# Kernel optimization log

Hardware: AMD Instinct MI355X
Metric: run time of the kernel (lower is better)

Reference implementation:

```python
import jax, jax.numpy as jnp
import numpy as np

N_NODES = 100000
N_EDGES = 1600000
IN_FEATS = 256
OUT_FEATS = 128


def setup_inputs() -> dict:
    key = jax.random.key(0)
    k1, k2, k3, k4, k5 = jax.random.split(key, 5)
    x = jax.random.normal(k1, (N_NODES, IN_FEATS), dtype=jnp.float32)
    edge_row = jax.random.randint(k2, (N_EDGES,), 0, N_NODES, dtype=jnp.int64 if jax.config.jax_enable_x64 else jnp.int32)
    edge_col = jax.random.randint(k3, (N_EDGES,), 0, N_NODES, dtype=jnp.int64 if jax.config.jax_enable_x64 else jnp.int32)
    edge_val = jax.random.uniform(k4, (N_EDGES,), dtype=jnp.float32)
    # xavier_uniform-like init for weight
    limit = float(np.sqrt(6.0 / (IN_FEATS + OUT_FEATS)))
    weight = jax.random.uniform(k5, (IN_FEATS, OUT_FEATS), dtype=jnp.float32, minval=-limit, maxval=limit)
    b = jnp.zeros((OUT_FEATS,), dtype=jnp.float32)
    return {"x": x, "edge_row": edge_row, "edge_col": edge_col, "edge_val": edge_val, "weight": weight, "b": b}


def reference(x, edge_row, edge_col, edge_val, weight, b):
    # sup = input @ weight : [N, out_feats]
    sup = x @ weight
    # out = spmm(adj, sup): gather source rows, scale by edge value, scatter-add to dest
    msgs = edge_val[:, None] * sup[edge_col]          # [E, out_feats]
    out = jax.ops.segment_sum(msgs, edge_row, num_segments=N_NODES)  # [N, out_feats]
    return out + b
```

## Files before the change

kernel.cpp:

```cpp
#include <hip/hip_runtime.h>


#define K_FEATS 256
#define N_FEATS 128
#define BSHIFT 7
#define BROWS 128
#define BCAP 3072
#define CHUNK 8192
#define EPT 32
#define RMOD 5

typedef __attribute__((ext_vector_type(8))) short short8;
typedef __attribute__((ext_vector_type(4))) float float4v;

__device__ __forceinline__ unsigned short f2bf(float f) {
    unsigned int u = __float_as_uint(f);
    unsigned int r = u + 0x7FFF + ((u >> 16) & 1);
    return (unsigned short)(r >> 16);
}

__global__ __launch_bounds__(256) void prep_w(const float* __restrict__ w,
                                              unsigned short* __restrict__ wt) {
    int n = blockIdx.x;
    int k = threadIdx.x;
    wt[n * K_FEATS + k] = f2bf(w[k * N_FEATS + n]);
}

__global__ __launch_bounds__(256) void zero_ints(int* __restrict__ p, int n) {
    int i = blockIdx.x * 256 + threadIdx.x;
    if (i < n) p[i] = 0;
}

__global__ __launch_bounds__(256) void gemm_partition(
        const float* __restrict__ x, const unsigned short* __restrict__ wt,
        unsigned short* __restrict__ sup, int M, int NT,
        const int* __restrict__ erow, const int* __restrict__ ecol,
        const float* __restrict__ eval_, int* __restrict__ bcur,
        int2* __restrict__ tmp, int E, int NB, int NCH) {
    __shared__ int hist[1024];
    __shared__ int cur[1024];
    const int g   = blockIdx.x;
    const int tid = threadIdx.x;

    if (g % RMOD == 0) {
        int pid = g / RMOD;
        if (pid >= NCH) return;
        const long e0 = (long)pid * CHUNK;

        for (int i = tid; i < NB; i += 256) hist[i] = 0;
        __syncthreads();

        int rows[EPT];
#pragma unroll
        for (int i = 0; i < EPT; i++) {
            long e = e0 + tid + i * 256;
            int r = -1;
            if (e < E) {
                r = erow[e];
                atomicAdd(&hist[r >> BSHIFT], 1);
            }
            rows[i] = r;
        }
        __syncthreads();

        for (int i = tid; i < NB; i += 256) {
            int c = hist[i];
            cur[i] = c ? atomicAdd(&bcur[i], c) : 0;
        }
        __syncthreads();

#pragma unroll
        for (int i = 0; i < EPT; i++) {
            long e = e0 + tid + i * 256;
            if (e >= E) continue;
            int r = rows[i];
            int b = r >> BSHIFT;
            int p = atomicAdd(&cur[b], 1);
            if (p < BCAP)
                tmp[(long)b * BCAP + p] = make_int2(((r & (BROWS - 1)) << 17) | ecol[e],
                                                    __float_as_int(eval_[e]));
        }
        return;
    }

    int tile = g - g / RMOD - 1;
    if (tile >= NT) return;

    const int wv   = tid >> 6;
    const int lane = tid & 63;
    const int l15  = lane & 15;
    const int quad = lane >> 4;
    const int row0 = tile * 128 + wv * 32;

    float4v acc[2][8];
#pragma unroll
    for (int mt = 0; mt < 2; mt++)
#pragma unroll
        for (int nt = 0; nt < 8; nt++) acc[mt][nt] = (float4v)(0.f);

#pragma unroll 2
    for (int k0 = 0; k0 < K_FEATS; k0 += 32) {
        short8 afrag[2];
#pragma unroll
        for (int mt = 0; mt < 2; mt++) {
            int grow = row0 + mt * 16 + l15;
            float4 a0 = make_float4(0.f, 0.f, 0.f, 0.f);
            float4 a1 = make_float4(0.f, 0.f, 0.f, 0.f);
            if (grow < M) {
                const float* p = x + (long)grow * K_FEATS + k0 + quad * 8;
                a0 = *(const float4*)p;
                a1 = *(const float4*)(p + 4);
            }
            short8 af;
            af[0] = (short)f2bf(a0.x); af[1] = (short)f2bf(a0.y);
            af[2] = (short)f2bf(a0.z); af[3] = (short)f2bf(a0.w);
            af[4] = (short)f2bf(a1.x); af[5] = (short)f2bf(a1.y);
            af[6] = (short)f2bf(a1.z); af[7] = (short)f2bf(a1.w);
            afrag[mt] = af;
        }
        short8 bfrag[8];
#pragma unroll
        for (int nt = 0; nt < 8; nt++) {
            bfrag[nt] = *(const short8*)(wt + (nt * 16 + l15) * K_FEATS + k0 + quad * 8);
        }
#pragma unroll
        for (int mt = 0; mt < 2; mt++)
#pragma unroll
            for (int nt = 0; nt < 8; nt++)
                acc[mt][nt] = __builtin_amdgcn_mfma_f32_16x16x32_bf16(
                    afrag[mt], bfrag[nt], acc[mt][nt], 0, 0, 0);
    }

#pragma unroll
    for (int mt = 0; mt < 2; mt++) {
#pragma unroll
        for (int reg = 0; reg < 4; reg++) {
            int grow = row0 + mt * 16 + quad * 4 + reg;
            if (grow < M) {
#pragma unroll
                for (int nt = 0; nt < 8; nt++) {
                    sup[(long)grow * N_FEATS + nt * 16 + l15] = f2bf(acc[mt][nt][reg]);
                }
            }
        }
    }
}

__global__ __launch_bounds__(1024) void bucket_scan(const int* __restrict__ bcnt,
                                                    int* __restrict__ bbase,
                                                    int* __restrict__ off0,
                                                    int NB, int M) {
    __shared__ int sm[1024];
    int t = threadIdx.x;
    int v = 0;
    if (t < NB) { v = bcnt[t]; if (v > BCAP) v = BCAP; }
    sm[t] = v;
    __syncthreads();
#pragma unroll
    for (int s = 1; s < 1024; s <<= 1) {
        int a = (t >= s) ? sm[t - s] : 0;
        __syncthreads();
        sm[t] += a;
        __syncthreads();
    }
    if (t < NB) bbase[t] = sm[t] - v;
    if (t == 1023) off0[M] = sm[1023];
}

__global__ __launch_bounds__(256) void bucket_to_sorted(const int* __restrict__ bcnt,
                                                        const int* __restrict__ bbase,
                                                        const int2* __restrict__ tmp,
                                                        int* __restrict__ off0,
                                                        int2* __restrict__ sedge, int M) {
    __shared__ int hist[BROWS];
    __shared__ int cur[BROWS];
    const int b   = blockIdx.x;
    const int tid = threadIdx.x;
    const int row0 = b << BSHIFT;

    if (tid < BROWS) hist[tid] = 0;
    __syncthreads();

    int cnt = bcnt[b];
    if (cnt > BCAP) cnt = BCAP;
    const int2* t = tmp + (long)b * BCAP;

    for (int i = tid; i < cnt; i += 256)
        atomicAdd(&hist[(unsigned)t[i].x >> 17], 1);
    __syncthreads();

    if (tid < BROWS) cur[tid] = hist[tid];
    __syncthreads();
#pragma unroll
    for (int s = 1; s < BROWS; s <<= 1) {
        int v = 0;
        if (tid >= s && tid < BROWS) v = cur[tid - s];
        __syncthreads();
        if (tid < BROWS) cur[tid] += v;
        __syncthreads();
    }

    const int base = bbase[b];
    if (tid < BROWS) {
        int start = base + cur[tid] - hist[tid];
        cur[tid] = start;
        if (row0 + tid < M) off0[row0 + tid] = start;
    }
    __syncthreads();

    for (int i = tid; i < cnt; i += 256) {
        int2 e = t[i];
        int rl = (unsigned)e.x >> 17;
        int p = atomicAdd(&cur[rl], 1);
        sedge[p] = make_int2(e.x & 0x1FFFF, e.y);
    }
}

__global__ __launch_bounds__(256) void gcn_spmm(const int* __restrict__ off0,
                                                const int2* __restrict__ sedge,
                                                const unsigned short* __restrict__ sup,
                                                const float* __restrict__ b,
                                                float* __restrict__ out, int M) {
    int row  = blockIdx.x * 4 + (threadIdx.x >> 6);
    if (row >= M) return;
    int lane = threadIdx.x & 63;
    int half = lane >> 5;
    int l31  = lane & 31;
    int s = off0[row], e = off0[row + 1];
    const uint2* sup64 = (const uint2*)sup;

    float4v acc = (float4v)(0.f);
    int base = s;
    for (; base + 8 <= e; base += 8) {
        int2 ed[4];
#pragma unroll
        for (int u = 0; u < 4; u++) ed[u] = sedge[base + half + 2 * u];
        uint2 g[4];
#pragma unroll
        for (int u = 0; u < 4; u++) g[u] = sup64[(long)ed[u].x * 32 + l31];
#pragma unroll
        for (int u = 0; u < 4; u++) {
            float v = __int_as_float(ed[u].y);
            acc.x += v * __uint_as_float(g[u].x << 16);
            acc.y += v * __uint_as_float(g[u].x & 0xFFFF0000u);
            acc.z += v * __uint_as_float(g[u].y << 16);
            acc.w += v * __uint_as_float(g[u].y & 0xFFFF0000u);
        }
    }
    for (int i = base + half; i < e; i += 2) {
        int2 ed = sedge[i];
        uint2 g = sup64[(long)ed.x * 32 + l31];
        float v = __int_as_float(ed.y);
        acc.x += v * __uint_as_float(g.x << 16);
        acc.y += v * __uint_as_float(g.x & 0xFFFF0000u);
        acc.z += v * __uint_as_float(g.y << 16);
        acc.w += v * __uint_as_float(g.y & 0xFFFF0000u);
    }

    acc.x += __shfl_xor(acc.x, 32);
    acc.y += __shfl_xor(acc.y, 32);
    acc.z += __shfl_xor(acc.z, 32);
    acc.w += __shfl_xor(acc.w, 32);

    if (half == 0) {
        float4v bb = ((const float4v*)b)[l31];
        acc += bb;
        *(float4v*)(out + (long)row * N_FEATS + l31 * 4) = acc;
    }
}

extern "C" void kernel_launch(void* const* d_in, const int* in_sizes, int n_in,
                              void* d_out, int out_size, void* d_ws, size_t ws_size,
                              hipStream_t stream) {
    const float* x     = (const float*)d_in[0];
    const int*   erow  = (const int*)d_in[1];
    const int*   ecol  = (const int*)d_in[2];
    const float* eval_ = (const float*)d_in[3];
    const float* w     = (const float*)d_in[4];
    const float* b     = (const float*)d_in[5];
    float* out = (float*)d_out;

    const int M  = in_sizes[0] / K_FEATS;
    const int E  = in_sizes[1];
    const int NB = (M + BROWS - 1) >> BSHIFT;
    const int NT = (M + 127) / 128;
    const int NCH = (E + CHUNK - 1) / CHUNK;

    size_t o_sup   = 0;
    size_t o_wt    = o_sup   + (((size_t)M * N_FEATS * 2 + 15) & ~15ul);
    size_t o_off0  = o_wt    + (size_t)K_FEATS * N_FEATS * 2;
    size_t o_bcur  = o_off0  + (((size_t)(M + 1) * 4 + 15) & ~15ul);
    size_t o_bbase = o_bcur  + (((size_t)NB * 4 + 15) & ~15ul);
    size_t o_tmp   = o_bbase + (((size_t)NB * 4 + 15) & ~15ul);
    size_t o_edge  = o_tmp   + ((size_t)NB * BCAP * 8);

    unsigned short* sup   = (unsigned short*)((char*)d_ws + o_sup);
    unsigned short* wt    = (unsigned short*)((char*)d_ws + o_wt);
    int*            off0  = (int*)((char*)d_ws + o_off0);
    int*            bcur  = (int*)((char*)d_ws + o_bcur);
    int*            bbase = (int*)((char*)d_ws + o_bbase);
    int2*           tmp   = (int2*)((char*)d_ws + o_tmp);
    int2*           sedge = (int2*)((char*)d_ws + o_edge);

    prep_w<<<N_FEATS, 256, 0, stream>>>(w, wt);
    zero_ints<<<(NB + 255) / 256, 256, 0, stream>>>(bcur, NB);

    int nblk = NT + NCH;
    gemm_partition<<<nblk, 256, 0, stream>>>(x, wt, sup, M, NT,
                                             erow, ecol, eval_, bcur, tmp, E, NB, NCH);

    bucket_scan<<<1, 1024, 0, stream>>>(bcur, bbase, off0, NB, M);
    bucket_to_sorted<<<NB, 256, 0, stream>>>(bcur, bbase, tmp, off0, sedge, M);

    gcn_spmm<<<(M + 3) / 4, 256, 0, stream>>>(off0, sedge, sup, b, out, M);
}
```

Baseline: 329.3 us.

## Replace bucketed two-pass CSR build with per-row histogram, scan, and atomic scatter

Replaces the row-bucket partitioning (LDS histogram, bucket temp buffer, per-bucket local sort) with a per-row global atomic histogram computed alongside the GEMM, a two-kernel prefix scan, and a direct atomic scatter into CSR order. This drops the intermediate bucket buffer and its extra read/write pass, but adds global atomics on 100k counters and non-deterministic edge order within rows. The GEMM also prefetches the next K-slice of x one iteration ahead and uses the packed v_cvt_pk_bf16_f32 instruction for bf16 conversion. Weight prep and counter zeroing are merged into one launch.

```diff
diff --git a/kernel.cpp b/kernel.cpp
--- a/kernel.cpp
+++ b/kernel.cpp
@@ -3,9 +3,6 @@
 
 #define K_FEATS 256
 #define N_FEATS 128
-#define BSHIFT 7
-#define BROWS 128
-#define BCAP 3072
 #define CHUNK 8192
 #define EPT 32
 #define RMOD 5
@@ -19,26 +16,29 @@
     return (unsigned short)(r >> 16);
 }
 
-__global__ __launch_bounds__(256) void prep_w(const float* __restrict__ w,
-                                              unsigned short* __restrict__ wt) {
-    int n = blockIdx.x;
-    int k = threadIdx.x;
-    wt[n * K_FEATS + k] = f2bf(w[k * N_FEATS + n]);
-}
-
-__global__ __launch_bounds__(256) void zero_ints(int* __restrict__ p, int n) {
-    int i = blockIdx.x * 256 + threadIdx.x;
-    if (i < n) p[i] = 0;
-}
-
-__global__ __launch_bounds__(256) void gemm_partition(
+__device__ __forceinline__ unsigned int cvt_pk_bf16(float lo, float hi) {
+    unsigned int r;
+    asm("v_cvt_pk_bf16_f32 %0, %1, %2" : "=v"(r) : "v"(lo), "v"(hi));
+    return r;
+}
+
+__global__ __launch_bounds__(256) void prep_zero(const float* __restrict__ w,
+                                                 unsigned short* __restrict__ wt,
+                                                 int* __restrict__ rcnt, int M) {
+    int g = blockIdx.x;
+    if (g < N_FEATS) {
+        int k = threadIdx.x;
+        wt[g * K_FEATS + k] = f2bf(w[k * N_FEATS + g]);
+        return;
+    }
+    int i = (g - N_FEATS) * 256 + threadIdx.x;
+    if (i < M) rcnt[i] = 0;
+}
+
+__global__ __launch_bounds__(256) void gemm_hist(
         const float* __restrict__ x, const unsigned short* __restrict__ wt,
         unsigned short* __restrict__ sup, int M, int NT,
-        const int* __restrict__ erow, const int* __restrict__ ecol,
-        const float* __restrict__ eval_, int* __restrict__ bcur,
-        int2* __restrict__ tmp, int E, int NB, int NCH) {
-    __shared__ int hist[1024];
-    __shared__ int cur[1024];
+        const int* __restrict__ erow, int* __restrict__ rcnt, int E, int NCH) {
     const int g   = blockIdx.x;
     const int tid = threadIdx.x;
 
@@ -46,39 +46,10 @@
         int pid = g / RMOD;
         if (pid >= NCH) return;
         const long e0 = (long)pid * CHUNK;
-
-        for (int i = tid; i < NB; i += 256) hist[i] = 0;
-        __syncthreads();
-
-        int rows[EPT];
 #pragma unroll
         for (int i = 0; i < EPT; i++) {
             long e = e0 + tid + i * 256;
-            int r = -1;
-            if (e < E) {
-                r = erow[e];
-                atomicAdd(&hist[r >> BSHIFT], 1);
-            }
-            rows[i] = r;
-        }
-        __syncthreads();
-
-        for (int i = tid; i < NB; i += 256) {
-            int c = hist[i];
-            cur[i] = c ? atomicAdd(&bcur[i], c) : 0;
-        }
-        __syncthreads();
-
-#pragma unroll
-        for (int i = 0; i < EPT; i++) {
-            long e = e0 + tid + i * 256;
-            if (e >= E) continue;
-            int r = rows[i];
-            int b = r >> BSHIFT;
-            int p = atomicAdd(&cur[b], 1);
-            if (p < BCAP)
-                tmp[(long)b * BCAP + p] = make_int2(((r & (BROWS - 1)) << 17) | ecol[e],
-                                                    __float_as_int(eval_[e]));
+            if (e < E) atomicAdd(&rcnt[erow[e]], 1);
         }
         return;
     }
@@ -98,30 +69,49 @@
 #pragma unroll
         for (int nt = 0; nt < 8; nt++) acc[mt][nt] = (float4v)(0.f);
 
+    float4 ca[2][2];
+#pragma unroll
+    for (int mt = 0; mt < 2; mt++) {
+        int grow = row0 + mt * 16 + l15;
+        ca[mt][0] = make_float4(0.f, 0.f, 0.f, 0.f);
+        ca[mt][1] = make_float4(0.f, 0.f, 0.f, 0.f);
+        if (grow < M) {
+            const float* p = x + (long)grow * K_FEATS + quad * 8;
+            ca[mt][0] = *(const float4*)p;
+            ca[mt][1] = *(const float4*)(p + 4);
+        }
+    }
+
 #pragma unroll 2
     for (int k0 = 0; k0 < K_FEATS; k0 += 32) {
-        short8 afrag[2];
-#pragma unroll
-        for (int mt = 0; mt < 2; mt++) {
-            int grow = row0 + mt * 16 + l15;
-            float4 a0 = make_float4(0.f, 0.f, 0.f, 0.f);
-            float4 a1 = make_float4(0.f, 0.f, 0.f, 0.f);
-            if (grow < M) {
-                const float* p = x + (long)grow * K_FEATS + k0 + quad * 8;
-                a0 = *(const float4*)p;
-                a1 = *(const float4*)(p + 4);
-            }
-            short8 af;
-            af[0] = (short)f2bf(a0.x); af[1] = (short)f2bf(a0.y);
-            af[2] = (short)f2bf(a0.z); af[3] = (short)f2bf(a0.w);
-            af[4] = (short)f2bf(a1.x); af[5] = (short)f2bf(a1.y);
-            af[6] = (short)f2bf(a1.z); af[7] = (short)f2bf(a1.w);
-            afrag[mt] = af;
-        }
         short8 bfrag[8];
 #pragma unroll
         for (int nt = 0; nt < 8; nt++) {
             bfrag[nt] = *(const short8*)(wt + (nt * 16 + l15) * K_FEATS + k0 + quad * 8);
+        }
+        float4 na[2][2];
+        if (k0 + 32 < K_FEATS) {
+#pragma unroll
+            for (int mt = 0; mt < 2; mt++) {
+                int grow = row0 + mt * 16 + l15;
+                na[mt][0] = make_float4(0.f, 0.f, 0.f, 0.f);
+                na[mt][1] = make_float4(0.f, 0.f, 0.f, 0.f);
+                if (grow < M) {
+                    const float* p = x + (long)grow * K_FEATS + (k0 + 32) + quad * 8;
+                    na[mt][0] = *(const float4*)p;
+                    na[mt][1] = *(const float4*)(p + 4);
+                }
+            }
+        }
+        short8 afrag[2];
+#pragma unroll
+        for (int mt = 0; mt < 2; mt++) {
+            union { short8 s; uint4 u; } cv;
+            cv.u.x = cvt_pk_bf16(ca[mt][0].x, ca[mt][0].y);
+            cv.u.y = cvt_pk_bf16(ca[mt][0].z, ca[mt][0].w);
+            cv.u.z = cvt_pk_bf16(ca[mt][1].x, ca[mt][1].y);
+            cv.u.w = cvt_pk_bf16(ca[mt][1].z, ca[mt][1].w);
+            afrag[mt] = cv.s;
         }
 #pragma unroll
         for (int mt = 0; mt < 2; mt++)
@@ -129,6 +119,11 @@
             for (int nt = 0; nt < 8; nt++)
                 acc[mt][nt] = __builtin_amdgcn_mfma_f32_16x16x32_bf16(
                     afrag[mt], bfrag[nt], acc[mt][nt], 0, 0, 0);
+#pragma unroll
+        for (int mt = 0; mt < 2; mt++) {
+            ca[mt][0] = na[mt][0];
+            ca[mt][1] = na[mt][1];
+        }
     }
 
 #pragma unroll
@@ -146,73 +141,87 @@
     }
 }
 
-__global__ __launch_bounds__(1024) void bucket_scan(const int* __restrict__ bcnt,
-                                                    int* __restrict__ bbase,
-                                                    int* __restrict__ off0,
-                                                    int NB, int M) {
-    __shared__ int sm[1024];
-    int t = threadIdx.x;
-    int v = 0;
-    if (t < NB) { v = bcnt[t]; if (v > BCAP) v = BCAP; }
-    sm[t] = v;
+__global__ __launch_bounds__(256) void scan_partial(const int* __restrict__ rcnt,
+                                                    int* __restrict__ bsum, int M) {
+    __shared__ int sm[256];
+    const int blk = blockIdx.x, t = threadIdx.x;
+    const int base = blk * 1024 + t * 4;
+    int s = 0;
+#pragma unroll
+    for (int j = 0; j < 4; j++) {
+        int i = base + j;
+        if (i < M) s += rcnt[i];
+    }
+    sm[t] = s;
     __syncthreads();
-#pragma unroll
-    for (int s = 1; s < 1024; s <<= 1) {
-        int a = (t >= s) ? sm[t - s] : 0;
+    for (int st = 128; st > 0; st >>= 1) {
+        if (t < st) sm[t] += sm[t + st];
+        __syncthreads();
+    }
+    if (t == 0) bsum[blk] = sm[0];
+}
+
+__global__ __launch_bounds__(256) void scan_final(const int* __restrict__ rcnt,
+                                                  const int* __restrict__ bsum,
+                                                  int* __restrict__ off0,
+                                                  int* __restrict__ cur, int M, int NB1) {
+    __shared__ int pb[128];
+    __shared__ int sm[256];
+    const int blk = blockIdx.x, t = threadIdx.x;
+
+    if (t < 128) pb[t] = (t < NB1) ? bsum[t] : 0;
+    __syncthreads();
+    for (int st = 1; st < 128; st <<= 1) {
+        int v = 0;
+        if (t >= st && t < 128) v = pb[t - st];
+        __syncthreads();
+        if (t < 128) pb[t] += v;
+        __syncthreads();
+    }
+    const int blockBase = (blk == 0) ? 0 : pb[blk - 1];
+
+    const int base = blk * 1024 + t * 4;
+    int v[4];
+    int s = 0;
+#pragma unroll
+    for (int j = 0; j < 4; j++) {
+        int i = base + j;
+        v[j] = (i < M) ? rcnt[i] : 0;
+        s += v[j];
+    }
+    sm[t] = s;
+    __syncthreads();
+    for (int st = 1; st < 256; st <<= 1) {
+        int a = 0;
+        if (t >= st) a = sm[t - st];
         __syncthreads();
         sm[t] += a;
         __syncthreads();
     }
-    if (t < NB) bbase[t] = sm[t] - v;
-    if (t == 1023) off0[M] = sm[1023];
-}
-
-__global__ __launch_bounds__(256) void bucket_to_sorted(const int* __restrict__ bcnt,
-                                                        const int* __restrict__ bbase,
-                                                        const int2* __restrict__ tmp,
-                                                        int* __restrict__ off0,
-                                                        int2* __restrict__ sedge, int M) {
-    __shared__ int hist[BROWS];
-    __shared__ int cur[BROWS];
-    const int b   = blockIdx.x;
-    const int tid = threadIdx.x;
-    const int row0 = b << BSHIFT;
-
-    if (tid < BROWS) hist[tid] = 0;
-    __syncthreads();
-
-    int cnt = bcnt[b];
-    if (cnt > BCAP) cnt = BCAP;
-    const int2* t = tmp + (long)b * BCAP;
-
-    for (int i = tid; i < cnt; i += 256)
-        atomicAdd(&hist[(unsigned)t[i].x >> 17], 1);
-    __syncthreads();
-
-    if (tid < BROWS) cur[tid] = hist[tid];
-    __syncthreads();
-#pragma unroll
-    for (int s = 1; s < BROWS; s <<= 1) {
-        int v = 0;
-        if (tid >= s && tid < BROWS) v = cur[tid - s];
-        __syncthreads();
-        if (tid < BROWS) cur[tid] += v;
-        __syncthreads();
-    }
-
-    const int base = bbase[b];
-    if (tid < BROWS) {
-        int start = base + cur[tid] - hist[tid];
-        cur[tid] = start;
-        if (row0 + tid < M) off0[row0 + tid] = start;
-    }
-    __syncthreads();
-
-    for (int i = tid; i < cnt; i += 256) {
-        int2 e = t[i];
-        int rl = (unsigned)e.x >> 17;
-        int p = atomicAdd(&cur[rl], 1);
-        sedge[p] = make_int2(e.x & 0x1FFFF, e.y);
+    int tb = blockBase + ((t == 0) ? 0 : sm[t - 1]);
+#pragma unroll
+    for (int j = 0; j < 4; j++) {
+        int i = base + j;
+        if (i < M) {
+            off0[i] = tb;
+            cur[i]  = tb;
+            tb += v[j];
+            if (i == M - 1) off0[M] = tb;
+        }
+    }
+}
+
+__global__ __launch_bounds__(256) void csr_scatter(const int* __restrict__ erow,
+                                                   const int* __restrict__ ecol,
+                                                   const float* __restrict__ eval_,
+                                                   int* __restrict__ cur,
+                                                   int2* __restrict__ sedge, int E) {
+    const int gid = blockIdx.x * 256 + threadIdx.x;
+    const int T   = gridDim.x * 256;
+    for (int e = gid; e < E; e += T) {
+        int r = erow[e];
+        int p = atomicAdd(&cur[r], 1);
+        sedge[p] = make_int2(ecol[e], __float_as_int(eval_[e]));
     }
 }
 
@@ -280,37 +289,36 @@
     const float* b     = (const float*)d_in[5];
     float* out = (float*)d_out;
 
-    const int M  = in_sizes[0] / K_FEATS;
-    const int E  = in_sizes[1];
-    const int NB = (M + BROWS - 1) >> BSHIFT;
-    const int NT = (M + 127) / 128;
+    const int M   = in_sizes[0] / K_FEATS;
+    const int E   = in_sizes[1];
+    const int NT  = (M + 127) / 128;
     const int NCH = (E + CHUNK - 1) / CHUNK;
-
-    size_t o_sup   = 0;
-    size_t o_wt    = o_sup   + (((size_t)M * N_FEATS * 2 + 15) & ~15ul);
-    size_t o_off0  = o_wt    + (size_t)K_FEATS * N_FEATS * 2;
-    size_t o_bcur  = o_off0  + (((size_t)(M + 1) * 4 + 15) & ~15ul);
-    size_t o_bbase = o_bcur  + (((size_t)NB * 4 + 15) & ~15ul);
-    size_t o_tmp   = o_bbase + (((size_t)NB * 4 + 15) & ~15ul);
-    size_t o_edge  = o_tmp   + ((size_t)NB * BCAP * 8);
-
-    unsigned short* sup   = (unsigned short*)((char*)d_ws + o_sup);
-    unsigned short* wt    = (unsigned short*)((char*)d_ws + o_wt);
-    int*            off0  = (int*)((char*)d_ws + o_off0);
-    int*            bcur  = (int*)((char*)d_ws + o_bcur);
-    int*            bbase = (int*)((char*)d_ws + o_bbase);
-    int2*           tmp   = (int2*)((char*)d_ws + o_tmp);
+    const int NB1 = (M + 1023) / 1024;
+
+    size_t o_sup  = 0;
+    size_t o_wt   = o_sup  + (((size_t)M * N_FEATS * 2 + 15) & ~15ul);
+    size_t o_off0 = o_wt   + (size_t)K_FEATS * N_FEATS * 2;
+    size_t o_rcnt = o_off0 + (((size_t)(M + 1) * 4 + 15) & ~15ul);
+    size_t o_cur  = o_rcnt + (((size_t)M * 4 + 15) & ~15ul);
+    size_t o_bsum = o_cur  + (((size_t)M * 4 + 15) & ~15ul);
+    size_t o_edge = o_bsum + (((size_t)NB1 * 4 + 15) & ~15ul);
+
+    unsigned short* sup  = (unsigned short*)((char*)d_ws + o_sup);
+    unsigned short* wt   = (unsigned short*)((char*)d_ws + o_wt);
+    int*            off0 = (int*)((char*)d_ws + o_off0);
+    int*            rcnt = (int*)((char*)d_ws + o_rcnt);
+    int*            cur  = (int*)((char*)d_ws + o_cur);
+    int*            bsum = (int*)((char*)d_ws + o_bsum);
     int2*           sedge = (int2*)((char*)d_ws + o_edge);
 
-    prep_w<<<N_FEATS, 256, 0, stream>>>(w, wt);
-    zero_ints<<<(NB + 255) / 256, 256, 0, stream>>>(bcur, NB);
-
-    int nblk = NT + NCH;
-    gemm_partition<<<nblk, 256, 0, stream>>>(x, wt, sup, M, NT,
-                                             erow, ecol, eval_, bcur, tmp, E, NB, NCH);
-
-    bucket_scan<<<1, 1024, 0, stream>>>(bcur, bbase, off0, NB, M);
-    bucket_to_sorted<<<NB, 256, 0, stream>>>(bcur, bbase, tmp, off0, sedge, M);
+    prep_zero<<<N_FEATS + (M + 255) / 256, 256, 0, stream>>>(w, wt, rcnt, M);
+
+    gemm_hist<<<NT + NCH, 256, 0, stream>>>(x, wt, sup, M, NT, erow, rcnt, E, NCH);
+
+    scan_partial<<<NB1, 256, 0, stream>>>(rcnt, bsum, M);
+    scan_final<<<NB1, 256, 0, stream>>>(rcnt, bsum, off0, cur, M, NB1);
+
+    csr_scatter<<<(E + 2047) / 2048, 256, 0, stream>>>(erow, ecol, eval_, cur, sedge, E);
 
     gcn_spmm<<<(M + 3) / 4, 256, 0, stream>>>(off0, sedge, sup, b, out, M);
 }
```

New measurement: 447.7 us. 1.36x slower.

## Fuse bucket scan, local sort and SpMM into one per-bucket kernel

Applied to the files above, without the earlier changes.

Replaces the global bucket scan, the bucket-to-sorted pass and the separate SpMM kernel with a single kernel per 128-row bucket. Each block counting-sorts its edges into shared memory (24 KB LDS) and then runs the gather-scale-sum directly from LDS. This removes two launches, the global sorted-edge write and re-read, and the offset array. The cost is fewer blocks (about 782 of them, each with 4 waves looping over 32 rows), so there is less parallelism to hide gather latency, and occupancy is limited by the LDS footprint.

```diff
diff --git a/kernel.cpp b/kernel.cpp
--- a/kernel.cpp
+++ b/kernel.cpp
@@ -6,6 +6,7 @@
 #define BSHIFT 7
 #define BROWS 128
 #define BCAP 3072
+#define STASH 12
 #define CHUNK 8192
 #define EPT 32
 #define RMOD 5
@@ -146,47 +147,38 @@
     }
 }
 
-__global__ __launch_bounds__(1024) void bucket_scan(const int* __restrict__ bcnt,
-                                                    int* __restrict__ bbase,
-                                                    int* __restrict__ off0,
-                                                    int NB, int M) {
-    __shared__ int sm[1024];
-    int t = threadIdx.x;
-    int v = 0;
-    if (t < NB) { v = bcnt[t]; if (v > BCAP) v = BCAP; }
-    sm[t] = v;
-    __syncthreads();
-#pragma unroll
-    for (int s = 1; s < 1024; s <<= 1) {
-        int a = (t >= s) ? sm[t - s] : 0;
-        __syncthreads();
-        sm[t] += a;
-        __syncthreads();
-    }
-    if (t < NB) bbase[t] = sm[t] - v;
-    if (t == 1023) off0[M] = sm[1023];
-}
-
-__global__ __launch_bounds__(256) void bucket_to_sorted(const int* __restrict__ bcnt,
-                                                        const int* __restrict__ bbase,
-                                                        const int2* __restrict__ tmp,
-                                                        int* __restrict__ off0,
-                                                        int2* __restrict__ sedge, int M) {
+__global__ __launch_bounds__(256) void bucket_spmm(const int* __restrict__ bcnt,
+                                                   const int2* __restrict__ tmp,
+                                                   const unsigned short* __restrict__ sup,
+                                                   const float* __restrict__ b,
+                                                   float* __restrict__ out, int M) {
     __shared__ int hist[BROWS];
+    __shared__ int rs[BROWS];
     __shared__ int cur[BROWS];
-    const int b   = blockIdx.x;
-    const int tid = threadIdx.x;
-    const int row0 = b << BSHIFT;
+    __shared__ __align__(16) int2 se[BCAP];
+    const int bkt  = blockIdx.x;
+    const int tid  = threadIdx.x;
+    const int wv   = tid >> 6;
+    const int lane = tid & 63;
+    const int row0 = bkt << BSHIFT;
 
     if (tid < BROWS) hist[tid] = 0;
     __syncthreads();
 
-    int cnt = bcnt[b];
+    int cnt = bcnt[bkt];
     if (cnt > BCAP) cnt = BCAP;
-    const int2* t = tmp + (long)b * BCAP;
-
-    for (int i = tid; i < cnt; i += 256)
-        atomicAdd(&hist[(unsigned)t[i].x >> 17], 1);
+    const int2* t = tmp + (long)bkt * BCAP;
+
+    int2 stash[STASH];
+#pragma unroll
+    for (int j = 0; j < STASH; j++) {
+        int i = tid + j * 256;
+        if (i < cnt) {
+            int2 e = t[i];
+            stash[j] = e;
+            atomicAdd(&hist[(unsigned)e.x >> 17], 1);
+        }
+    }
     __syncthreads();
 
     if (tid < BROWS) cur[tid] = hist[tid];
@@ -199,73 +191,74 @@
         if (tid < BROWS) cur[tid] += v;
         __syncthreads();
     }
-
-    const int base = bbase[b];
     if (tid < BROWS) {
-        int start = base + cur[tid] - hist[tid];
+        int start = cur[tid] - hist[tid];
+        rs[tid]  = start;
         cur[tid] = start;
-        if (row0 + tid < M) off0[row0 + tid] = start;
-    }
-    __syncthreads();
-
-    for (int i = tid; i < cnt; i += 256) {
-        int2 e = t[i];
-        int rl = (unsigned)e.x >> 17;
-        int p = atomicAdd(&cur[rl], 1);
-        sedge[p] = make_int2(e.x & 0x1FFFF, e.y);
-    }
-}
-
-__global__ __launch_bounds__(256) void gcn_spmm(const int* __restrict__ off0,
-                                                const int2* __restrict__ sedge,
-                                                const unsigned short* __restrict__ sup,
-                                                const float* __restrict__ b,
-                                                float* __restrict__ out, int M) {
-    int row  = blockIdx.x * 4 + (threadIdx.x >> 6);
-    if (row >= M) return;
-    int lane = threadIdx.x & 63;
-    int half = lane >> 5;
-    int l31  = lane & 31;
-    int s = off0[row], e = off0[row + 1];
+    }
+    __syncthreads();
+
+#pragma unroll
+    for (int j = 0; j < STASH; j++) {
+        int i = tid + j * 256;
+        if (i < cnt) {
+            int2 e = stash[j];
+            int rl = (unsigned)e.x >> 17;
+            int p = atomicAdd(&cur[rl], 1);
+            se[p] = make_int2(e.x & 0x1FFFF, e.y);
+        }
+    }
+    __syncthreads();
+
+    const int half = lane >> 5;
+    const int l31  = lane & 31;
     const uint2* sup64 = (const uint2*)sup;
-
-    float4v acc = (float4v)(0.f);
-    int base = s;
-    for (; base + 8 <= e; base += 8) {
-        int2 ed[4];
-#pragma unroll
-        for (int u = 0; u < 4; u++) ed[u] = sedge[base + half + 2 * u];
-        uint2 g[4];
-#pragma unroll
-        for (int u = 0; u < 4; u++) g[u] = sup64[(long)ed[u].x * 32 + l31];
-#pragma unroll
-        for (int u = 0; u < 4; u++) {
-            float v = __int_as_float(ed[u].y);
-            acc.x += v * __uint_as_float(g[u].x << 16);
-            acc.y += v * __uint_as_float(g[u].x & 0xFFFF0000u);
-            acc.z += v * __uint_as_float(g[u].y << 16);
-            acc.w += v * __uint_as_float(g[u].y & 0xFFFF0000u);
-        }
-    }
-    for (int i = base + half; i < e; i += 2) {
-        int2 ed = sedge[i];
-        uint2 g = sup64[(long)ed.x * 32 + l31];
-        float v = __int_as_float(ed.y);
-        acc.x += v * __uint_as_float(g.x << 16);
-        acc.y += v * __uint_as_float(g.x & 0xFFFF0000u);
-        acc.z += v * __uint_as_float(g.y << 16);
-        acc.w += v * __uint_as_float(g.y & 0xFFFF0000u);
-    }
-
-    acc.x += __shfl_xor(acc.x, 32);
-    acc.y += __shfl_xor(acc.y, 32);
-    acc.z += __shfl_xor(acc.z, 32);
-    acc.w += __shfl_xor(acc.w, 32);
-
-    if (half == 0) {
-        float4v bb = ((const float4v*)b)[l31];
-        acc += bb;
-        *(float4v*)(out + (long)row * N_FEATS + l31 * 4) = acc;
+    const float4v bb = ((const float4v*)b)[l31];
+
+    for (int rr = 0; rr < 32; rr++) {
+        int r    = wv * 32 + rr;
+        int grow = row0 + r;
+        if (grow >= M) break;
+        int s  = rs[r];
+        int e2 = s + hist[r];
+
+        float4v acc = (float4v)(0.f);
+        int base = s;
+        for (; base + 8 <= e2; base += 8) {
+            int2 ed[4];
+#pragma unroll
+            for (int u = 0; u < 4; u++) ed[u] = se[base + half + 2 * u];
+            uint2 g[4];
+#pragma unroll
+            for (int u = 0; u < 4; u++) g[u] = sup64[(long)ed[u].x * 32 + l31];
+#pragma unroll
+            for (int u = 0; u < 4; u++) {
+                float v = __int_as_float(ed[u].y);
+                acc.x += v * __uint_as_float(g[u].x << 16);
+                acc.y += v * __uint_as_float(g[u].x & 0xFFFF0000u);
+                acc.z += v * __uint_as_float(g[u].y << 16);
+                acc.w += v * __uint_as_float(g[u].y & 0xFFFF0000u);
+            }
+        }
+        for (int i = base + half; i < e2; i += 2) {
+            int2 ed = se[i];
+            uint2 g = sup64[(long)ed.x * 32 + l31];
+            float v = __int_as_float(ed.y);
+            acc.x += v * __uint_as_float(g.x << 16);
+            acc.y += v * __uint_as_float(g.x & 0xFFFF0000u);
+            acc.z += v * __uint_as_float(g.y << 16);
+            acc.w += v * __uint_as_float(g.y & 0xFFFF0000u);
+        }
+
+        acc.x += __shfl_xor(acc.x, 32);
+        acc.y += __shfl_xor(acc.y, 32);
+        acc.z += __shfl_xor(acc.z, 32);
+        acc.w += __shfl_xor(acc.w, 32);
+
+        if (half == 0) {
+            float4v o = acc + bb;
+            *(float4v*)(out + (long)grow * N_FEATS + l31 * 4) = o;
+        }
     }
 }
 
@@ -280,37 +273,27 @@
     const float* b     = (const float*)d_in[5];
     float* out = (float*)d_out;
 
-    const int M  = in_sizes[0] / K_FEATS;
-    const int E  = in_sizes[1];
-    const int NB = (M + BROWS - 1) >> BSHIFT;
-    const int NT = (M + 127) / 128;
+    const int M   = in_sizes[0] / K_FEATS;
+    const int E   = in_sizes[1];
+    const int NB  = (M + BROWS - 1) >> BSHIFT;
+    const int NT  = (M + 127) / 128;
     const int NCH = (E + CHUNK - 1) / CHUNK;
 
-    size_t o_sup   = 0;
-    size_t o_wt    = o_sup   + (((size_t)M * N_FEATS * 2 + 15) & ~15ul);
-    size_t o_off0  = o_wt    + (size_t)K_FEATS * N_FEATS * 2;
-    size_t o_bcur  = o_off0  + (((size_t)(M + 1) * 4 + 15) & ~15ul);
-    size_t o_bbase = o_bcur  + (((size_t)NB * 4 + 15) & ~15ul);
-    size_t o_tmp   = o_bbase + (((size_t)NB * 4 + 15) & ~15ul);
-    size_t o_edge  = o_tmp   + ((size_t)NB * BCAP * 8);
-
-    unsigned short* sup   = (unsigned short*)((char*)d_ws + o_sup);
-    unsigned short* wt    = (unsigned short*)((char*)d_ws + o_wt);
-    int*            off0  = (int*)((char*)d_ws + o_off0);
-    int*            bcur  = (int*)((char*)d_ws + o_bcur);
-    int*            bbase = (int*)((char*)d_ws + o_bbase);
-    int2*           tmp   = (int2*)((char*)d_ws + o_tmp);
-    int2*           sedge = (int2*)((char*)d_ws + o_edge);
+    size_t o_sup  = 0;
+    size_t o_wt   = o_sup  + (((size_t)M * N_FEATS * 2 + 15) & ~15ul);
+    size_t o_bcur = o_wt   + (size_t)K_FEATS * N_FEATS * 2;
+    size_t o_tmp  = o_bcur + (((size_t)NB * 4 + 15) & ~15ul);
+
+    unsigned short* sup  = (unsigned short*)((char*)d_ws + o_sup);
+    unsigned short* wt   = (unsigned short*)((char*)d_ws + o_wt);
+    int*            bcur = (int*)((char*)d_ws + o_bcur);
+    int2*           tmp  = (int2*)((char*)d_ws + o_tmp);
 
     prep_w<<<N_FEATS, 256, 0, stream>>>(w, wt);
     zero_ints<<<(NB + 255) / 256, 256, 0, stream>>>(bcur, NB);
 
-    int nblk = NT + NCH;
-    gemm_partition<<<nblk, 256, 0, stream>>>(x, wt, sup, M, NT,
-                                             erow, ecol, eval_, bcur, tmp, E, NB, NCH);
-
-    bucket_scan<<<1, 1024, 0, stream>>>(bcur, bbase, off0, NB, M);
-    bucket_to_sorted<<<NB, 256, 0, stream>>>(bcur, bbase, tmp, off0, sedge, M);
-
-    gcn_spmm<<<(M + 3) / 4, 256, 0, stream>>>(off0, sedge, sup, b, out, M);
-}
+    gemm_partition<<<NT + NCH, 256, 0, stream>>>(x, wt, sup, M, NT,
+                                                 erow, ecol, eval_, bcur, tmp, E, NB, NCH);
+
+    bucket_spmm<<<NB, 256, 0, stream>>>(bcur, tmp, sup, b, out, M);
+}
```

New measurement: 317.5 us. 3.6% less time.
